# Kernel tuning notes

Measured on AMD Instinct MI355X. Metric: run time of the kernel, lower is better.

Reference implementation:

```python
import jax, jax.numpy as jnp
import numpy as np

B, N_ATOMS = 64, 127            # graphs, atoms per graph (uniform)
L = N_ATOMS + 1                 # +1 cls token
D_MODEL, NHEAD, NUM_LAYERS, D_FF = 1024, 16, 8, 3072
HEAD_DIM = D_MODEL // NHEAD
MAX_TOKENS = 131                # 121 + 10
NEIGH_VOCAB = 14 + 3            # max_neighbors + 3
DIST_VOCAB = 83 + 3             # max_distance + 3
EPS = 1e-5


def _dist_bins():
    # short_cutoff=0.9, long_cutoff=5.0, precision=0.05; first 3 edges overridden
    b = np.arange(0.9 - 3 * 0.05, 5.0, 0.05)
    b[:3] = [-1.0, 0.0, 0.01]
    return jnp.asarray(b, jnp.float32)  # len 85 -> digitize indices in [0, 85]


def _layer_norm(x, g, b):
    m = jnp.mean(x, -1, keepdims=True)
    v = jnp.var(x, -1, keepdims=True)
    return (x - m) * jax.lax.rsqrt(v + EPS) * g + b


def setup_inputs() -> dict:
    key = jax.random.key(0)
    ks = jax.random.split(key, 16)
    s = 0.02
    z = jax.random.randint(ks[0], (B * N_ATOMS,), 0, 119)
    hgs = jax.random.randint(ks[1], (B * N_ATOMS,), 0, 15)
    pos = jax.random.normal(ks[2], (B * N_ATOMS, 3), jnp.float32) * 3.0
    batch = jnp.repeat(jnp.arange(B, dtype=jnp.int64), N_ATOMS)
    atoms_emb = (jax.random.normal(ks[3], (MAX_TOKENS, D_MODEL), jnp.float32) * s).at[0].set(0.0)  # padding_idx=0
    neigh_emb = (jax.random.normal(ks[4], (NEIGH_VOCAB, D_MODEL), jnp.float32) * s).at[0].set(0.0)
    dist_emb = jax.random.normal(ks[5], (DIST_VOCAB, NHEAD), jnp.float32) * s  # row 0 forced to -inf in reference
    Wqkv = jax.random.normal(ks[6], (D_MODEL, 3 * D_MODEL), jnp.float32) * s
    bqkv = jnp.zeros((3 * D_MODEL,), jnp.float32)
    Wo = jax.random.normal(ks[7], (D_MODEL, D_MODEL), jnp.float32) * s
    bo = jnp.zeros((D_MODEL,), jnp.float32)
    W1 = jax.random.normal(ks[8], (D_MODEL, D_FF), jnp.float32) * s
    b1f = jnp.zeros((D_FF,), jnp.float32)
    W2 = jax.random.normal(ks[9], (D_FF, D_MODEL), jnp.float32) * s
    b2f = jnp.zeros((D_MODEL,), jnp.float32)
    ln1_g = jnp.ones((D_MODEL,), jnp.float32); ln1_b = jnp.zeros((D_MODEL,), jnp.float32)
    ln2_g = jnp.ones((D_MODEL,), jnp.float32); ln2_b = jnp.zeros((D_MODEL,), jnp.float32)
    return dict(z=z, hgs=hgs, pos=pos, batch=batch, atoms_emb=atoms_emb, neigh_emb=neigh_emb,
                dist_emb=dist_emb, Wqkv=Wqkv, bqkv=bqkv, Wo=Wo, bo=bo,
                W1=W1, b1f=b1f, W2=W2, b2f=b2f,
                ln1_g=ln1_g, ln1_b=ln1_b, ln2_g=ln2_g, ln2_b=ln2_b)


def reference(z, hgs, pos, batch, atoms_emb, neigh_emb, dist_emb,
              Wqkv, bqkv, Wo, bo, W1, b1f, W2, b2f, ln1_g, ln1_b, ln2_g, ln2_b):
    # batch is uniform (N_ATOMS per graph, sorted), so per-graph batching == reshape
    zb = z.reshape(B, N_ATOMS).astype(jnp.int32) + 2
    hb = hgs.reshape(B, N_ATOMS).astype(jnp.int32) + 2
    atoms = jnp.concatenate([jnp.ones((B, 1), jnp.int32), zb], axis=1)        # cls token = 1
    neighbors = jnp.concatenate([jnp.zeros((B, 1), jnp.int32), hb], axis=1)   # cls neighbors = 0

    p = pos.reshape(B, N_ATOMS, 3)
    dist = jnp.sqrt(jnp.sum((p[:, None, :, :] - p[:, :, None, :]) ** 2, axis=-1))  # (B,n,n)
    didx = jnp.digitize(dist, _dist_bins()).astype(jnp.int32)                      # self-loop -> 2
    distances = jnp.ones((B, L, L), jnp.int32).at[:, 1:, 1:].set(didx)             # cls row/col = 1

    # neg_inf_idx=0 padding mask row (unused here since no padding -> indices >= 1)
    w_d = dist_emb.at[0].set(-jnp.inf)
    d_mask = w_d[distances].transpose(0, 3, 1, 2)  # (B, H, L, L)

    x = atoms_emb[atoms] + neigh_emb[neighbors]    # (B, L, D)
    scale = 1.0 / jnp.sqrt(jnp.float32(HEAD_DIM))
    for _ in range(NUM_LAYERS):  # shared weights + shared attention bias
        qkv = x @ Wqkv + bqkv
        q, k, v = jnp.split(qkv, 3, axis=-1)
        q = q.reshape(B, L, NHEAD, HEAD_DIM)
        k = k.reshape(B, L, NHEAD, HEAD_DIM)
        v = v.reshape(B, L, NHEAD, HEAD_DIM)
        scores = jnp.einsum('blhd,bmhd->bhlm', q, k) * scale + d_mask
        a = jax.nn.softmax(scores, axis=-1)
        o = jnp.einsum('bhlm,bmhd->blhd', a, v).reshape(B, L, D_MODEL) @ Wo + bo
        x = _layer_norm(x + o, ln1_g, ln1_b)                      # post-norm (norm_first=False)
        h = jax.nn.gelu(x @ W1 + b1f, approximate=False) @ W2 + b2f
        x = _layer_norm(x + h, ln2_g, ln2_b)
    return x[:, 0]  # cls embedding, (B, D_MODEL)
```

## Files before the change

kernel.cpp:

```cpp
#include <hip/hip_runtime.h>
#include <cstdint>
#include <math.h>

typedef unsigned short u16;
typedef __attribute__((ext_vector_type(4))) float f32x4;
typedef __attribute__((ext_vector_type(8))) __bf16 bf16x8;
typedef __attribute__((ext_vector_type(8))) short short8;

typedef __attribute__((address_space(1))) void g_void;
typedef __attribute__((address_space(3))) void l_void;

__device__ __forceinline__ u16 f2bf(float f) {
  uint32_t u = __builtin_bit_cast(uint32_t, f);
  u += 0x7FFFu + ((u >> 16) & 1u);
  return (u16)(u >> 16);
}
__device__ __forceinline__ float bf2f(u16 h) {
  uint32_t u = ((uint32_t)h) << 16;
  return __builtin_bit_cast(float, u);
}

__device__ __forceinline__ void gload16(const void* g, void* l) {
  __builtin_amdgcn_global_load_lds((g_void*)g, (l_void*)l, 16, 0, 0);
}

__device__ __forceinline__ float gelu_exact(float x) {
  float a = x * 0.70710678118654752f;
  float s = fabsf(a);
  float t = __builtin_amdgcn_rcpf(fmaf(0.3275911f, s, 1.0f));
  float p = fmaf(fmaf(fmaf(fmaf(1.061405429f, t, -1.453152027f), t, 1.421413741f), t,
                      -0.284496736f), t, 0.254829592f);
  p *= t;
  float e = __expf(-s * s);
  float er = fmaf(-p, e, 1.0f);
  er = copysignf(er, a);
  return 0.5f * x * (1.0f + er);
}

__global__ void transpose_w(const float* __restrict__ W, u16* __restrict__ Wt, int K, int N) {
  __shared__ float t[32][33];
  const int nb = blockIdx.x * 32, kb = blockIdx.y * 32;
  const int tx = threadIdx.x, ty = threadIdx.y;
#pragma unroll
  for (int i = 0; i < 32; i += 8)
    t[ty + i][tx] = W[(size_t)(kb + ty + i) * N + nb + tx];
  __syncthreads();
#pragma unroll
  for (int i = 0; i < 32; i += 8)
    Wt[(size_t)(nb + ty + i) * K + kb + tx] = f2bf(t[tx][ty + i]);
}

__global__ void embed_k(const int* __restrict__ z, const int* __restrict__ hgs,
                        const float* __restrict__ ae, const float* __restrict__ ne,
                        u16* __restrict__ xb) {
  const int row = blockIdx.x;
  const int b = row >> 7, tl = row & 127;
  int ia = 1, in_ = 0;
  if (tl > 0) { ia = z[b * 127 + tl - 1] + 2; in_ = hgs[b * 127 + tl - 1] + 2; }
  const float* ar = ae + (size_t)ia * 1024;
  const float* nr = ne + (size_t)in_ * 1024;
  for (int c = threadIdx.x; c < 1024; c += 256)
    xb[(size_t)row * 1024 + c] = f2bf(ar[c] + nr[c]);
}

__global__ void mask_k(const float* __restrict__ pos, const float* __restrict__ demb,
                       u16* __restrict__ mask) {
  __shared__ float edges[85];
  __shared__ float dhT[16 * 86];
  const int blk = blockIdx.x;
  const int b = blk >> 7, lk = blk & 127;
  const int lq = threadIdx.x;
  if (lq < 85) {
    double e = 0.75 + 0.05 * (double)lq;
    float ef = (float)e;
    if (lq == 0) ef = -1.0f; else if (lq == 1) ef = 0.0f; else if (lq == 2) ef = 0.01f;
    edges[lq] = ef;
  }
  for (int i = lq; i < 16 * 86; i += 128) {
    const int h = i / 86, c = i - h * 86;
    float v = (c == 0) ? -INFINITY : demb[c * 16 + h] * 8.0f;
    dhT[i] = v;
  }
  __syncthreads();
  int c;
  if (lq == 0 || lk == 0) {
    c = 1;
  } else {
    const float* pi = pos + ((size_t)b * 127 + lq - 1) * 3;
    const float* pj = pos + ((size_t)b * 127 + lk - 1) * 3;
    const float dx = pi[0] - pj[0], dy = pi[1] - pj[1], dz = pi[2] - pj[2];
    const float d = sqrtf(dx * dx + dy * dy + dz * dz);
    int cnt = 0;
#pragma unroll
    for (int k2 = 0; k2 < 85; ++k2) cnt += (edges[k2] <= d) ? 1 : 0;
    c = cnt;
  }
#pragma unroll
  for (int h = 0; h < 16; ++h)
    mask[((size_t)(b * 16 + h) << 14) + lk * 128 + lq] = f2bf(dhT[h * 86 + c]);
}

template <int MODE>
__launch_bounds__(512, 4)
__global__ void gemmS(const u16* __restrict__ A, const u16* __restrict__ Bt,
                      const float* __restrict__ bias,
                      u16* __restrict__ O0, u16* __restrict__ O1, u16* __restrict__ O2,
                      int N, int K) {
  extern __shared__ char lds[];
  constexpr int SLAB = 24576;
  const int tid = threadIdx.x;
  const int w = tid >> 6, l = tid & 63;
  const int wr = w >> 1, wc = w & 1;
  const int nwg = gridDim.x;
  const int wg = (blockIdx.x & 7) * (nwg >> 3) + (blockIdx.x >> 3);
  const int ntn = N >> 7;
  const int bm = wg / ntn, bn = wg - (wg / ntn) * ntn;
  const int NT = K >> 5;

  const int colc = ((((l & 3) << 4) ^ (((l >> 2) & 8) << 2)) >> 1);
  const u16* Ag = A + (size_t)(bm * 256 + w * 16 + (l >> 2)) * K + colc;
  const u16* Bg = Bt + (size_t)(bn * 128 + w * 16 + (l >> 2)) * K + colc;
  const int ldst = w << 10;

  auto stage = [&](int t, char* buf) {
    const int kb = t << 5;
    gload16(Ag + kb, buf + ldst);
    gload16(Ag + (size_t)128 * K + kb, buf + 8192 + ldst);
    gload16(Bg + kb, buf + 16384 + ldst);
  };

  const int lo = ((l & 15) << 6) + (((l >> 4) << 4) ^ ((l & 8) << 2));

  f32x4 acc[4][4];
#pragma unroll
  for (int m = 0; m < 4; ++m)
#pragma unroll
    for (int n = 0; n < 4; ++n) acc[m][n] = f32x4{0.f, 0.f, 0.f, 0.f};

  char* p0 = lds;
  char* p1 = lds + SLAB;
  char* p2 = lds + 2 * SLAB;

  stage(0, p0);
  stage(1, p1);
  asm volatile("s_waitcnt vmcnt(3)" ::: "memory");
  __builtin_amdgcn_s_barrier();

  for (int t = 0; t < NT; ++t) {
    if (t + 2 < NT) stage(t + 2, p2);
    const char* ab = p0 + (wr << 12);
    const char* bb = p0 + 16384 + (wc << 12);
    bf16x8 af[4], bf[4];
#pragma unroll
    for (int m = 0; m < 4; ++m) af[m] = *(const bf16x8*)(ab + (m << 10) + lo);
#pragma unroll
    for (int n = 0; n < 4; ++n) bf[n] = *(const bf16x8*)(bb + (n << 10) + lo);
    __builtin_amdgcn_s_setprio(1);
#pragma unroll
    for (int m = 0; m < 4; ++m)
#pragma unroll
      for (int n = 0; n < 4; ++n)
        acc[m][n] = __builtin_amdgcn_mfma_f32_16x16x32_bf16(af[m], bf[n], acc[m][n], 0, 0, 0);
    __builtin_amdgcn_s_setprio(0);
    if (t + 2 < NT) asm volatile("s_waitcnt vmcnt(3)" ::: "memory");
    else            asm volatile("s_waitcnt vmcnt(0)" ::: "memory");
    __builtin_amdgcn_s_barrier();
    char* tmp = p0; p0 = p1; p1 = p2; p2 = tmp;
  }

  const int fr = l & 15, fq = l >> 4;
  const int colb = bn * 128 + wc * 64;
  const int rowb = bm * 256 + wr * 64;
  float bv[4];
#pragma unroll
  for (int n = 0; n < 4; ++n) bv[n] = bias[colb + n * 16 + fr];
  const int region = colb >> 10;

#pragma unroll
  for (int m = 0; m < 4; ++m) {
#pragma unroll
    for (int n = 0; n < 4; ++n) {
      const int col = colb + n * 16 + fr;
      if (MODE == 0 && region == 2) {
        const int row0_ = rowb + m * 16 + fq * 4;
        const int bI = row0_ >> 7, tl0 = row0_ & 127;
        const int c = col & 1023, h = c >> 6, d = c & 63;
        ushort4 pk;
        pk.x = f2bf(acc[m][n][0] + bv[n]);
        pk.y = f2bf(acc[m][n][1] + bv[n]);
        pk.z = f2bf(acc[m][n][2] + bv[n]);
        pk.w = f2bf(acc[m][n][3] + bv[n]);
        *(ushort4*)&O2[(((size_t)bI * 16 + h) * 64 + d) * 128 + tl0] = pk;
      } else {
#pragma unroll
        for (int j = 0; j < 4; ++j) {
          const int row = rowb + m * 16 + fq * 4 + j;
          float v = acc[m][n][j] + bv[n];
          if (MODE == 2) v = gelu_exact(v);
          if (MODE == 0) {
            const int bI = row >> 7, tl = row & 127;
            const int c = col & 1023, h = c >> 6, d = c & 63;
            if (region == 0) O0[(((size_t)bI * 16 + h) * 128 + tl) * 64 + d] = f2bf(v);
            else             O1[(((size_t)bI * 16 + h) * 128 + tl) * 64 + d] = f2bf(v);
          } else {
            O0[(size_t)row * N + col] = f2bf(v);
          }
        }
      }
    }
  }
}

__launch_bounds__(256, 2)
__global__ void gemm4r(const u16* __restrict__ A, const u16* __restrict__ Bt,
                       const float* __restrict__ bias, u16* __restrict__ O,
                       int N, int K) {
  extern __shared__ char lds[];
  const int tid = threadIdx.x;
  const int w = tid >> 6, l = tid & 63;
  const int wr = w >> 1, wc = w & 1;
  const int nwg = gridDim.x;
  const int wg = (blockIdx.x & 7) * (nwg >> 3) + (blockIdx.x >> 3);
  const int ntn = N >> 7;
  const int bm = wg / ntn, bn = wg - (wg / ntn) * ntn;
  const int NT = K >> 5;

  const int colc = ((((l & 3) << 4) ^ (((l >> 2) & 8) << 2)) >> 1);
  const u16* Ag = A + (size_t)(bm * 128 + w * 16 + (l >> 2)) * K + colc;
  const u16* Bg = Bt + (size_t)(bn * 128 + w * 16 + (l >> 2)) * K + colc;
  const int ldst = w << 10;

  auto stage = [&](int t) {
    char* buf = lds + ((t & 3) << 14);
    const int kb = t << 5;
    gload16(Ag + kb, buf + ldst);
    gload16(Ag + (size_t)64 * K + kb, buf + 4096 + ldst);
    gload16(Bg + kb, buf + 8192 + ldst);
    gload16(Bg + (size_t)64 * K + kb, buf + 12288 + ldst);
  };

  const int lo = ((l & 15) << 6) + (((l >> 4) << 4) ^ ((l & 8) << 2));

  f32x4 acc[4][4];
#pragma unroll
  for (int m = 0; m < 4; ++m)
#pragma unroll
    for (int n = 0; n < 4; ++n) acc[m][n] = f32x4{0.f, 0.f, 0.f, 0.f};

  auto compute = [&](int bi) {
    const char* ab = lds + (bi << 14) + (wr << 12);
    const char* bb = lds + (bi << 14) + 8192 + (wc << 12);
    bf16x8 af[4], bf[4];
#pragma unroll
    for (int m = 0; m < 4; ++m) af[m] = *(const bf16x8*)(ab + (m << 10) + lo);
#pragma unroll
    for (int n = 0; n < 4; ++n) bf[n] = *(const bf16x8*)(bb + (n << 10) + lo);
    __builtin_amdgcn_s_setprio(1);
#pragma unroll
    for (int m = 0; m < 4; ++m)
#pragma unroll
      for (int n = 0; n < 4; ++n)
        acc[m][n] = __builtin_amdgcn_mfma_f32_16x16x32_bf16(af[m], bf[n], acc[m][n], 0, 0, 0);
    __builtin_amdgcn_s_setprio(0);
  };

  stage(0); stage(1); stage(2);
  asm volatile("s_waitcnt vmcnt(8)" ::: "memory");
  __builtin_amdgcn_s_barrier();

  for (int t4 = 0; t4 + 4 < NT; t4 += 4) {
#pragma unroll
    for (int u = 0; u < 4; ++u) {
      stage(t4 + u + 3);
      compute(u);
      asm volatile("s_waitcnt vmcnt(8)" ::: "memory");
      __builtin_amdgcn_s_barrier();
    }
  }
  stage(NT - 1);
  compute(0);
  asm volatile("s_waitcnt vmcnt(8)" ::: "memory");
  __builtin_amdgcn_s_barrier();
  compute(1);
  asm volatile("s_waitcnt vmcnt(4)" ::: "memory");
  __builtin_amdgcn_s_barrier();
  compute(2);
  asm volatile("s_waitcnt vmcnt(0)" ::: "memory");
  __builtin_amdgcn_s_barrier();
  compute(3);

  const int fr = l & 15, fq = l >> 4;
  const int colb = bn * 128 + wc * 64;
  const int rowb = bm * 128 + wr * 64;
  float bv[4];
#pragma unroll
  for (int n = 0; n < 4; ++n) bv[n] = bias[colb + n * 16 + fr];
#pragma unroll
  for (int m = 0; m < 4; ++m)
#pragma unroll
    for (int n = 0; n < 4; ++n) {
      const int col = colb + n * 16 + fr;
#pragma unroll
      for (int j = 0; j < 4; ++j) {
        const int row = rowb + m * 16 + fq * 4 + j;
        O[(size_t)row * N + col] = f2bf(acc[m][n][j] + bv[n]);
      }
    }
}

__launch_bounds__(256)
__global__ void attn_kernel(const u16* __restrict__ Qg, const u16* __restrict__ Kg,
                            const u16* __restrict__ Vg,
                            const u16* __restrict__ mask,
                            u16* __restrict__ Og) {
  __shared__ u16 QK[2 * 128 * 64];
  __shared__ u16 Vt[64 * 128];
  const int tid = threadIdx.x;
  const int wv = tid >> 6;
  const int l = tid & 63;
  const int bh = blockIdx.x;
  const int b = bh >> 4;

  const char* Qs = (const char*)(Qg + (size_t)bh * 8192);
  const char* Ks = (const char*)(Kg + (size_t)bh * 8192);
  const char* Vs = (const char*)(Vg + (size_t)bh * 8192);
  char* QKb = (char*)QK;
  char* Vtb = (char*)Vt;
#pragma unroll
  for (int it = 0; it < 4; ++it) {
    const int r = it * 32 + (tid >> 3);
    const int cb = (tid & 7) * 16;
    const int sw = cb ^ ((r & 7) << 4);
    *(uint4*)(QKb + r * 128 + sw) = *(const uint4*)(Qs + r * 128 + cb);
    *(uint4*)(QKb + 16384 + r * 128 + sw) = *(const uint4*)(Ks + r * 128 + cb);
  }
#pragma unroll
  for (int it = 0; it < 4; ++it) {
    const int r = it * 16 + (tid >> 4);
    const int cb = (tid & 15) * 16;
    const int sw = cb ^ ((r & 7) << 4);
    *(uint4*)(Vtb + r * 256 + sw) = *(const uint4*)(Vs + r * 256 + cb);
  }

  const u16* m8 = mask + ((size_t)bh << 14);
  f32x4 s[2][8];
#pragma unroll
  for (int m = 0; m < 2; ++m) {
    const int r0 = wv * 32 + m * 16 + (l >> 4) * 4;
#pragma unroll
    for (int n = 0; n < 8; ++n) {
      const int col = n * 16 + (l & 15);
      const ushort4 mv = *(const ushort4*)(m8 + col * 128 + r0);
      s[m][n] = f32x4{bf2f(mv.x), bf2f(mv.y), bf2f(mv.z), bf2f(mv.w)};
    }
  }
  __syncthreads();

#pragma unroll
  for (int kk = 0; kk < 2; ++kk) {
    bf16x8 qa[2], kb[8];
#pragma unroll
    for (int m = 0; m < 2; ++m) {
      const int qr = wv * 32 + m * 16 + (l & 15);
      qa[m] = *(const bf16x8*)(QKb + qr * 128 + ((kk * 64 + (l >> 4) * 16) ^ ((qr & 7) << 4)));
    }
#pragma unroll
    for (int n = 0; n < 8; ++n) {
      const int kr = n * 16 + (l & 15);
      kb[n] = *(const bf16x8*)(QKb + 16384 + kr * 128 + ((kk * 64 + (l >> 4) * 16) ^ ((kr & 7) << 4)));
    }
#pragma unroll
    for (int m = 0; m < 2; ++m)
#pragma unroll
      for (int n = 0; n < 8; ++n)
        s[m][n] = __builtin_amdgcn_mfma_f32_16x16x32_bf16(qa[m], kb[n], s[m][n], 0, 0, 0);
  }

  float rinv[2][4];
#pragma unroll
  for (int m = 0; m < 2; ++m) {
#pragma unroll
    for (int j = 0; j < 4; ++j) {
      float vals[8];
#pragma unroll
      for (int n = 0; n < 8; ++n)
        vals[n] = s[m][n][j] * 0.125f;
      float mx = vals[0];
#pragma unroll
      for (int n = 1; n < 8; ++n) mx = fmaxf(mx, vals[n]);
#pragma unroll
      for (int o = 1; o < 16; o <<= 1) mx = fmaxf(mx, __shfl_xor(mx, o, 64));
      float sum = 0.f;
#pragma unroll
      for (int n = 0; n < 8; ++n) { vals[n] = expf(vals[n] - mx); sum += vals[n]; }
#pragma unroll
      for (int o = 1; o < 16; o <<= 1) sum += __shfl_xor(sum, o, 64);
      rinv[m][j] = 1.f / sum;
#pragma unroll
      for (int n = 0; n < 8; ++n) s[m][n][j] = vals[n];
    }
  }
  __syncthreads();
  char* Pb = QKb + wv * 8192;
#pragma unroll
  for (int m = 0; m < 2; ++m)
#pragma unroll
    for (int n = 0; n < 8; ++n)
#pragma unroll
      for (int j = 0; j < 4; ++j) {
        const int pr = m * 16 + (l >> 4) * 4 + j;
        const int pc = (n * 16 + (l & 15)) * 2;
        *(u16*)(Pb + pr * 256 + (pc ^ ((pr & 7) << 4))) = f2bf(s[m][n][j]);
      }

  f32x4 o_[2][4];
#pragma unroll
  for (int m = 0; m < 2; ++m)
#pragma unroll
    for (int n = 0; n < 4; ++n) o_[m][n] = f32x4{0.f, 0.f, 0.f, 0.f};
#pragma unroll
  for (int ks = 0; ks < 4; ++ks) {
    bf16x8 pa[2], vb[4];
#pragma unroll
    for (int m = 0; m < 2; ++m) {
      const int pr = m * 16 + (l & 15);
      pa[m] = *(const bf16x8*)(Pb + pr * 256 + ((ks * 64 + (l >> 4) * 16) ^ ((pr & 7) << 4)));
    }
#pragma unroll
    for (int n = 0; n < 4; ++n) {
      const int vr = n * 16 + (l & 15);
      vb[n] = *(const bf16x8*)(Vtb + vr * 256 + ((ks * 64 + (l >> 4) * 16) ^ ((vr & 7) << 4)));
    }
#pragma unroll
    for (int m = 0; m < 2; ++m)
#pragma unroll
      for (int n = 0; n < 4; ++n)
        o_[m][n] = __builtin_amdgcn_mfma_f32_16x16x32_bf16(pa[m], vb[n], o_[m][n], 0, 0, 0);
  }
  const int h = bh & 15;
#pragma unroll
  for (int m = 0; m < 2; ++m)
#pragma unroll
    for (int n = 0; n < 4; ++n)
#pragma unroll
      for (int j = 0; j < 4; ++j) {
        const int lo2 = wv * 32 + m * 16 + (l >> 4) * 4 + j;
        const int d = n * 16 + (l & 15);
        Og[((size_t)b * 128 + lo2) * 1024 + h * 64 + d] = f2bf(o_[m][n][j] * rinv[m][j]);
      }
}

__launch_bounds__(256)
__global__ void ln_res(u16* __restrict__ xb, const u16* __restrict__ o,
                       const float* __restrict__ gam, const float* __restrict__ bet,
                       float* __restrict__ cls_out) {
  const int row = blockIdx.x * 4 + (threadIdx.x >> 6);
  const int l = threadIdx.x & 63;
  const size_t base = (size_t)row * 1024 + l * 16;
  const int c0 = l * 16;
  float v[16], gv[16], bb[16];
  const short8 xa = *(const short8*)(xb + base);
  const short8 xc = *(const short8*)(xb + base + 8);
  const short8 oa = *(const short8*)(o + base);
  const short8 oc = *(const short8*)(o + base + 8);
#pragma unroll
  for (int i = 0; i < 4; ++i) {
    *(float4*)&gv[i * 4] = *(const float4*)(gam + c0 + i * 4);
    *(float4*)&bb[i * 4] = *(const float4*)(bet + c0 + i * 4);
  }
  float s = 0.f, sq = 0.f;
#pragma unroll
  for (int i = 0; i < 8; ++i) {
    v[i] = bf2f((u16)xa[i]) + bf2f((u16)oa[i]);
    v[i + 8] = bf2f((u16)xc[i]) + bf2f((u16)oc[i]);
  }
#pragma unroll
  for (int i = 0; i < 16; ++i) { s += v[i]; sq += v[i] * v[i]; }
#pragma unroll
  for (int off = 1; off < 64; off <<= 1) {
    s += __shfl_xor(s, off, 64);
    sq += __shfl_xor(sq, off, 64);
  }
  const float mean = s * (1.f / 1024.f);
  const float var = sq * (1.f / 1024.f) - mean * mean;
  const float rstd = rsqrtf(var + 1e-5f);
  short8 ra, rc;
#pragma unroll
  for (int i = 0; i < 8; ++i) {
    const float ya = (v[i] - mean) * rstd * gv[i] + bb[i];
    const float yc = (v[i + 8] - mean) * rstd * gv[i + 8] + bb[i + 8];
    ra[i] = (short)f2bf(ya);
    rc[i] = (short)f2bf(yc);
    if ((row & 127) == 0) {
      cls_out[(size_t)(row >> 7) * 1024 + c0 + i] = ya;
      cls_out[(size_t)(row >> 7) * 1024 + c0 + 8 + i] = yc;
    }
  }
  *(short8*)(xb + base) = ra;
  *(short8*)(xb + base + 8) = rc;
}

extern "C" void kernel_launch(void* const* d_in, const int* in_sizes, int n_in,
                              void* d_out, int out_size, void* d_ws, size_t ws_size,
                              hipStream_t stream) {
  const int* z = (const int*)d_in[0];
  const int* hgs = (const int*)d_in[1];
  const float* pos = (const float*)d_in[2];
  const float* atoms_emb = (const float*)d_in[4];
  const float* neigh_emb = (const float*)d_in[5];
  const float* dist_emb = (const float*)d_in[6];
  const float* Wqkv = (const float*)d_in[7];
  const float* bqkv = (const float*)d_in[8];
  const float* Wo = (const float*)d_in[9];
  const float* bo = (const float*)d_in[10];
  const float* W1 = (const float*)d_in[11];
  const float* b1f = (const float*)d_in[12];
  const float* W2 = (const float*)d_in[13];
  const float* b2f = (const float*)d_in[14];
  const float* ln1g = (const float*)d_in[15];
  const float* ln1b = (const float*)d_in[16];
  const float* ln2g = (const float*)d_in[17];
  const float* ln2b = (const float*)d_in[18];

  size_t off = 0;
  char* wsb = (char*)d_ws;
  auto alc = [&](size_t bytes) { void* p = wsb + off; off += (bytes + 255) & ~(size_t)255; return p; };
  u16* xb = (u16*)alc(8192ull * 1024 * 2);
  u16* q = (u16*)alc(8192ull * 1024 * 2);
  u16* k = (u16*)alc(8192ull * 1024 * 2);
  u16* v = (u16*)alc(8192ull * 1024 * 2);
  u16* proj = (u16*)alc(8192ull * 1024 * 2);
  u16* big = (u16*)alc(8192ull * 3072 * 2);
  u16* wqkvt = (u16*)alc(3072ull * 1024 * 2);
  u16* wot = (u16*)alc(1024ull * 1024 * 2);
  u16* w1t = (u16*)alc(3072ull * 1024 * 2);
  u16* w2t = (u16*)alc(1024ull * 3072 * 2);
  u16* mask = (u16*)alc(64ull * 16 * 128 * 128 * 2);

  hipFuncSetAttribute((const void*)gemmS<0>, hipFuncAttributeMaxDynamicSharedMemorySize, 73728);
  hipFuncSetAttribute((const void*)gemmS<2>, hipFuncAttributeMaxDynamicSharedMemorySize, 73728);
  hipFuncSetAttribute((const void*)gemm4r, hipFuncAttributeMaxDynamicSharedMemorySize, 65536);

  transpose_w<<<dim3(96, 32), dim3(32, 8), 0, stream>>>(Wqkv, wqkvt, 1024, 3072);
  transpose_w<<<dim3(32, 32), dim3(32, 8), 0, stream>>>(Wo, wot, 1024, 1024);
  transpose_w<<<dim3(96, 32), dim3(32, 8), 0, stream>>>(W1, w1t, 1024, 3072);
  transpose_w<<<dim3(32, 96), dim3(32, 8), 0, stream>>>(W2, w2t, 3072, 1024);
  embed_k<<<8192, 256, 0, stream>>>(z, hgs, atoms_emb, neigh_emb, xb);
  mask_k<<<8192, 128, 0, stream>>>(pos, dist_emb, mask);

  float* cls = (float*)d_out;
  for (int layer = 0; layer < 8; ++layer) {
    gemmS<0><<<768, 512, 73728, stream>>>(xb, wqkvt, bqkv, q, k, v, 3072, 1024);
    attn_kernel<<<1024, 256, 0, stream>>>(q, k, v, mask, big);
    gemm4r<<<512, 256, 65536, stream>>>(big, wot, bo, proj, 1024, 1024);
    ln_res<<<2048, 256, 0, stream>>>(xb, proj, ln1g, ln1b, cls);
    gemmS<2><<<768, 512, 73728, stream>>>(xb, w1t, b1f, big, nullptr, nullptr, 3072, 1024);
    gemm4r<<<512, 256, 65536, stream>>>(big, w2t, b2f, proj, 1024, 3072);
    ln_res<<<2048, 256, 0, stream>>>(xb, proj, ln2g, ln2b, cls);
  }
}
```

Before: 2.222 ms.

## Split GEMM k-step into two interleaved phases with staggered global loads

Each k-iteration of the bf16 GEMM main loop is split into two halves. The B-fragment LDS reads, the global-to-LDS prefetch issues and the MFMA batches are interleaved across the halves, with extra barriers and lgkmcnt waits, so memory issue spreads across the compute. The aim is better overlap of LDS and global traffic with the matrix cores, at the cost of three extra workgroup barriers per iteration.

```diff
diff --git a/kernel.cpp b/kernel.cpp
--- a/kernel.cpp
+++ b/kernel.cpp
@@ -122,13 +122,6 @@
   const u16* Bg = Bt + (size_t)(bn * 128 + w * 16 + (l >> 2)) * K + colc;
   const int ldst = w << 10;
 
-  auto stage = [&](int t, char* buf) {
-    const int kb = t << 5;
-    gload16(Ag + kb, buf + ldst);
-    gload16(Ag + (size_t)128 * K + kb, buf + 8192 + ldst);
-    gload16(Bg + kb, buf + 16384 + ldst);
-  };
-
   const int lo = ((l & 15) << 6) + (((l >> 4) << 4) ^ ((l & 8) << 2));
 
   f32x4 acc[4][4];
@@ -141,29 +134,55 @@
   char* p1 = lds + SLAB;
   char* p2 = lds + 2 * SLAB;
 
-  stage(0, p0);
-  stage(1, p1);
+  {
+    gload16(Ag + 0, p0 + ldst);
+    gload16(Ag + (size_t)128 * K + 0, p0 + 8192 + ldst);
+    gload16(Bg + 0, p0 + 16384 + ldst);
+    gload16(Ag + 32, p1 + ldst);
+    gload16(Ag + (size_t)128 * K + 32, p1 + 8192 + ldst);
+    gload16(Bg + 32, p1 + 16384 + ldst);
+  }
   asm volatile("s_waitcnt vmcnt(3)" ::: "memory");
   __builtin_amdgcn_s_barrier();
 
   for (int t = 0; t < NT; ++t) {
-    if (t + 2 < NT) stage(t + 2, p2);
+    const bool pre = (t + 2 < NT);
+    const int kb2 = (t + 2) << 5;
     const char* ab = p0 + (wr << 12);
     const char* bb = p0 + 16384 + (wc << 12);
     bf16x8 af[4], bf[4];
 #pragma unroll
     for (int m = 0; m < 4; ++m) af[m] = *(const bf16x8*)(ab + (m << 10) + lo);
 #pragma unroll
-    for (int n = 0; n < 4; ++n) bf[n] = *(const bf16x8*)(bb + (n << 10) + lo);
+    for (int n = 0; n < 2; ++n) bf[n] = *(const bf16x8*)(bb + (n << 10) + lo);
+    if (pre) {
+      gload16(Ag + kb2, p2 + ldst);
+      gload16(Ag + (size_t)128 * K + kb2, p2 + 8192 + ldst);
+    }
+    __builtin_amdgcn_s_barrier();
+    asm volatile("s_waitcnt lgkmcnt(0)" ::: "memory");
     __builtin_amdgcn_s_setprio(1);
 #pragma unroll
     for (int m = 0; m < 4; ++m)
 #pragma unroll
-      for (int n = 0; n < 4; ++n)
+      for (int n = 0; n < 2; ++n)
         acc[m][n] = __builtin_amdgcn_mfma_f32_16x16x32_bf16(af[m], bf[n], acc[m][n], 0, 0, 0);
     __builtin_amdgcn_s_setprio(0);
-    if (t + 2 < NT) asm volatile("s_waitcnt vmcnt(3)" ::: "memory");
-    else            asm volatile("s_waitcnt vmcnt(0)" ::: "memory");
+    __builtin_amdgcn_s_barrier();
+#pragma unroll
+    for (int n = 2; n < 4; ++n) bf[n] = *(const bf16x8*)(bb + (n << 10) + lo);
+    if (pre) gload16(Bg + kb2, p2 + 16384 + ldst);
+    __builtin_amdgcn_s_barrier();
+    asm volatile("s_waitcnt lgkmcnt(0)" ::: "memory");
+    __builtin_amdgcn_s_setprio(1);
+#pragma unroll
+    for (int m = 0; m < 4; ++m)
+#pragma unroll
+      for (int n = 2; n < 4; ++n)
+        acc[m][n] = __builtin_amdgcn_mfma_f32_16x16x32_bf16(af[m], bf[n], acc[m][n], 0, 0, 0);
+    __builtin_amdgcn_s_setprio(0);
+    if (pre) asm volatile("s_waitcnt vmcnt(3)" ::: "memory");
+    else     asm volatile("s_waitcnt vmcnt(0)" ::: "memory");
     __builtin_amdgcn_s_barrier();
     char* tmp = p0; p0 = p1; p1 = p2; p2 = tmp;
   }
```

New measurement: 2.190 ms, median of 3. No clear change (-1.5%).
